# Kernel tuning notes

Measured on AMD Instinct MI355X. Metric: run time of the kernel, lower is better.

## Reference

```python
import jax, jax.numpy as jnp
import numpy as np

K = 32        # num_classes
NQ = 16384    # num query samples
C = 512       # feature_dim
H_REF = 512   # refinement_net hidden
H_CONF = 256  # confidence_net hidden
NUM_STEPS = 3


def setup_inputs() -> dict:
    key = jax.random.key(0)
    ks = jax.random.split(key, 8)
    s = 0.02
    return {
        "prototypes": jax.random.normal(ks[0], (K, C), jnp.float32),
        "query_features": jax.random.normal(ks[1], (NQ, C), jnp.float32),
        "query_distances": jax.random.uniform(ks[2], (NQ, K), jnp.float32) * 10.0,
        "W1": jax.random.normal(ks[3], (2 * C, H_REF), jnp.float32) * s,
        "b1": jnp.zeros((H_REF,), jnp.float32),
        "W2": jax.random.normal(ks[4], (H_REF, C), jnp.float32) * s,
        "b2": jnp.zeros((C,), jnp.float32),
        "Wc1": jax.random.normal(ks[5], (2 * C, H_CONF), jnp.float32) * s,
        "bc1": jnp.zeros((H_CONF,), jnp.float32),
        "Wc2": jax.random.normal(ks[6], (H_CONF, 1), jnp.float32) * s,
        "bc2": jnp.zeros((1,), jnp.float32),
    }


def reference(prototypes, query_features, query_distances,
              W1, b1, W2, b2, Wc1, bc1, Wc2, bc2):
    # ---- refinement loop (3 steps, sequential in refined prototypes) ----
    refined = prototypes
    for step in range(NUM_STEPS):
        # soft assignments over classes; temperature = step + 1
        soft = jax.nn.softmax(-query_distances / (step + 1.0), axis=-1)  # (NQ, K)
        wsum = jnp.maximum(soft.sum(axis=0), 1e-6)                       # (K,)  clamp(min=1e-6)
        wmean = (soft.T @ query_features) / wsum[:, None]                # (K, C)
        concat = jnp.concatenate([refined, wmean], axis=-1)              # (K, 2C)
        h = jax.nn.relu(concat @ W1 + b1)                                # dropout is identity in eval
        refinement = h @ W2 + b2                                         # (K, C)
        refined = refined + 0.1 * refinement

    # ---- confidence scores: MLP on [proto, query] pairs, mean over queries ----
    # Split first-layer weight into proto half and query half to avoid
    # materializing the (K, NQ, 2C) concat explicitly (same math).
    Wp, Wq = Wc1[:C], Wc1[C:]
    hp = prototypes @ Wp          # (K, H_CONF)
    hq = query_features @ Wq      # (NQ, H_CONF)
    hidden = jax.nn.relu(hp[:, None, :] + hq[None, :, :] + bc1)  # (K, NQ, H_CONF)
    conf = jax.nn.sigmoid(hidden @ Wc2 + bc2)                    # (K, NQ, 1)
    confidence_scores = conf.reshape(K, -1).mean(axis=1)         # (K,)

    return refined, confidence_scores
```

## Files before the change

kernel.cpp:

```cpp
#include <hip/hip_runtime.h>

#define KP 32
#define NQg 16384
#define CD 512
#define HC 256
#define NS 3

typedef __attribute__((ext_vector_type(8))) short short8;
typedef __attribute__((ext_vector_type(4))) short short4_t;
typedef __attribute__((ext_vector_type(8))) __bf16 bf16x8;
typedef __attribute__((ext_vector_type(4))) float floatx4;

union S8B8 { short8 s; bf16x8 b; };

__device__ __forceinline__ short f2bf(float f) {
    union { float f; unsigned u; } v; v.f = f;
    unsigned r = v.u + 0x7fffu + ((v.u >> 16) & 1u);
    return (short)(r >> 16);
}
__device__ __forceinline__ float bf2f(short s) {
    union { unsigned u; float f; } v; v.u = ((unsigned)(unsigned short)s) << 16;
    return v.f;
}
__device__ __forceinline__ float bflo(unsigned u) { return __uint_as_float(u << 16); }
__device__ __forceinline__ float bfhi(unsigned u) { return __uint_as_float(u & 0xffff0000u); }

__global__ __launch_bounds__(256) void k_A(const float* __restrict__ qd,
                                           const float* __restrict__ W1, const float* __restrict__ W2,
                                           const float* __restrict__ Wc1, const float* __restrict__ proto,
                                           const float* __restrict__ qf,
                                           short* __restrict__ softT,
                                           short* __restrict__ W1p, short* __restrict__ W2p,
                                           short* __restrict__ wqp, float* __restrict__ refined,
                                           short* __restrict__ qf2b, float* __restrict__ wmean,
                                           int* __restrict__ bar, float* __restrict__ dout) {
    int tid = threadIdx.x;
    int bid = blockIdx.x;
    if (bid < 64) {
        int q = bid * 256 + tid;
        float d[32];
        const float4* p = (const float4*)(qd + (size_t)q * 32);
#pragma unroll
        for (int j = 0; j < 8; j++) {
            float4 v = p[j];
            d[4 * j] = v.x; d[4 * j + 1] = v.y; d[4 * j + 2] = v.z; d[4 * j + 3] = v.w;
        }
#pragma unroll
        for (int s = 0; s < 3; s++) {
            float inv = -1.0f / (float)(s + 1);
            float e[32];
            float sum = 0.f;
#pragma unroll
            for (int k = 0; k < 32; k++) { e[k] = __expf(d[k] * inv); sum += e[k]; }
            float r = 1.0f / sum;
#pragma unroll
            for (int k = 0; k < 32; k++)
                softT[(size_t)(s * 32 + k) * NQg + q] = f2bf(e[k] * r);
        }
        return;
    }
    if (bid < 3712) {
        if (bid == 64) {
            if (tid < 32) dout[16384 + tid] = 0.f;
            else if (tid < 40) bar[tid - 32] = 0;
        }
        int idx = (bid - 64) * 256 + tid;
        if (idx < 524288) {
            int k = idx >> 9, n = idx & 511;
            W1p[((size_t)(k >> 3) * 512 + n) * 8 + (k & 7)] = f2bf(W1[idx]);
        } else if (idx < 786432) {
            int j = idx - 524288;
            int k = j >> 9, n = j & 511;
            W2p[((size_t)(k >> 3) * 512 + n) * 8 + (k & 7)] = f2bf(W2[j]);
        } else if (idx < 917504) {
            int j = idx - 786432;
            int k = j >> 8, n = j & 255;
            wqp[((size_t)(k >> 3) * 256 + n) * 8 + (k & 7)] = f2bf(Wc1[(size_t)(512 + k) * 256 + n]);
        } else {
            int j = idx - 917504;
            refined[j] = proto[j];
        }
        return;
    }
    if (bid < 3904) {
        int idx = (bid - 3712) * 256 + tid;
        wmean[idx] = 0.f;
        return;
    }
    {
#pragma unroll
        for (int it = 0; it < 4; it++) {
            int j = (bid - 3904) * 1024 + it * 256 + tid;
            float4 v = *(const float4*)&qf[(size_t)j * 4];
            short4_t o;
            o[0] = f2bf(v.x); o[1] = f2bf(v.y); o[2] = f2bf(v.z); o[3] = f2bf(v.w);
            *(short4_t*)&qf2b[(size_t)j * 4] = o;
        }
    }
}

__global__ __launch_bounds__(256) void k_B(const short* __restrict__ qf2b,
                                           const short* __restrict__ softT,
                                           const short* __restrict__ wqp,
                                           float* __restrict__ wmean,
                                           short* __restrict__ hq_g,
                                           float* __restrict__ wsuminv,
                                           const float* __restrict__ proto,
                                           const float* __restrict__ Wc1,
                                           const float* __restrict__ bc1,
                                           float* __restrict__ hpb) {
    __shared__ short B_lds[128 * 40];
    int tid = threadIdx.x;
    int lane = tid & 63, w = tid >> 6;
    int ml = lane & 15, q8 = lane >> 4;

    if (blockIdx.x < 256) {
        int kc = blockIdx.x >> 2, ns = blockIdx.x & 3;
        int c0 = ns * 128;
        int qbase0 = kc * 256;
        int c_l = 2 * lane;
        int q_l = 8 * w;

        floatx4 acc[6][2];
#pragma unroll
        for (int mt = 0; mt < 6; mt++)
#pragma unroll
            for (int nt = 0; nt < 2; nt++) acc[mt][nt] = (floatx4){0.f, 0.f, 0.f, 0.f};

        for (int step = 0; step < 8; step++) {
            int qb = qbase0 + step * 32;
            short8 sA, sB;
#pragma unroll
            for (int i = 0; i < 8; i++) {
                unsigned u = *(const unsigned*)&qf2b[(size_t)(qb + q_l + i) * 512 + c0 + c_l];
                sA[i] = (short)(u & 0xffffu);
                sB[i] = (short)(u >> 16);
            }
            __syncthreads();
            *(short8*)&B_lds[c_l * 40 + q_l] = sA;
            *(short8*)&B_lds[(c_l + 1) * 40 + q_l] = sB;
            S8B8 a[6];
#pragma unroll
            for (int mt = 0; mt < 6; mt++)
                a[mt].s = *(const short8*)&softT[(size_t)(mt * 16 + ml) * NQg + qb + q8 * 8];
            __syncthreads();
#pragma unroll
            for (int nt = 0; nt < 2; nt++) {
                S8B8 b; b.s = *(short8*)&B_lds[(w * 32 + nt * 16 + ml) * 40 + q8 * 8];
#pragma unroll
                for (int mt = 0; mt < 6; mt++)
                    acc[mt][nt] = __builtin_amdgcn_mfma_f32_16x16x32_bf16(a[mt].b, b.b, acc[mt][nt], 0, 0, 0);
            }
        }
#pragma unroll
        for (int mt = 0; mt < 6; mt++) {
#pragma unroll
            for (int nt = 0; nt < 2; nt++) {
                int c = c0 + w * 32 + nt * 16 + ml;
#pragma unroll
                for (int r = 0; r < 4; r++) {
                    int m = mt * 16 + q8 * 4 + r;
                    atomicAdd(&wmean[(size_t)m * 512 + c], acc[mt][nt][r]);
                }
            }
        }
    } else if (blockIdx.x < 512) {
        int m0 = (blockIdx.x - 256) * 64;
        int n0 = w * 64;
        floatx4 acc[4][4];
#pragma unroll
        for (int mt = 0; mt < 4; mt++)
#pragma unroll
            for (int nt = 0; nt < 4; nt++) acc[mt][nt] = (floatx4){0.f, 0.f, 0.f, 0.f};

#pragma unroll 4
        for (int kc = 0; kc < 512; kc += 32) {
            S8B8 a[4], b[4];
#pragma unroll
            for (int mt = 0; mt < 4; mt++)
                a[mt].s = *(const short8*)&qf2b[(size_t)(m0 + mt * 16 + ml) * 512 + kc + q8 * 8];
#pragma unroll
            for (int nt = 0; nt < 4; nt++)
                b[nt].s = *(const short8*)&wqp[((size_t)((kc >> 3) + q8) * 256 + n0 + nt * 16 + ml) * 8];
#pragma unroll
            for (int mt = 0; mt < 4; mt++)
#pragma unroll
                for (int nt = 0; nt < 4; nt++)
                    acc[mt][nt] = __builtin_amdgcn_mfma_f32_16x16x32_bf16(a[mt].b, b[nt].b, acc[mt][nt], 0, 0, 0);
        }
#pragma unroll
        for (int mt = 0; mt < 4; mt++)
#pragma unroll
            for (int nt = 0; nt < 4; nt++) {
                int col = n0 + nt * 16 + ml;
#pragma unroll
                for (int r = 0; r < 4; r++) {
                    int row = m0 + mt * 16 + q8 * 4 + r;
                    hq_g[(size_t)row * 256 + col] = f2bf(acc[mt][nt][r]);
                }
            }
    } else if (blockIdx.x < 608) {
        float* red = (float*)B_lds;
        int sk = blockIdx.x - 512;
        const short* row = softT + (size_t)sk * NQg;
        float s = 0.f;
#pragma unroll
        for (int j = 0; j < 8; j++) {
            short8 v = *(const short8*)&row[j * 2048 + tid * 8];
#pragma unroll
            for (int i = 0; i < 8; i++) s += bf2f(v[i]);
        }
        red[tid] = s;
        __syncthreads();
        for (int off = 128; off > 0; off >>= 1) {
            if (tid < off) red[tid] += red[tid + off];
            __syncthreads();
        }
        if (tid == 0) wsuminv[sk] = 1.0f / fmaxf(red[0], 1e-6f);
    } else {
        int r = blockIdx.x - 608;
        const float* pr = proto + r * 512;
        const float* wc = Wc1 + tid;
        float a0 = 0.f, a1 = 0.f, a2 = 0.f, a3 = 0.f;
#pragma unroll 4
        for (int i = 0; i < 512; i += 4) {
            float4 p4 = *(const float4*)&pr[i];
            float w0 = wc[(size_t)i * 256];
            float w1 = wc[(size_t)(i + 1) * 256];
            float w2 = wc[(size_t)(i + 2) * 256];
            float w3 = wc[(size_t)(i + 3) * 256];
            a0 += p4.x * w0;
            a1 += p4.y * w1;
            a2 += p4.z * w2;
            a3 += p4.w * w3;
        }
        hpb[r * 256 + tid] = bc1[tid] + ((a0 + a1) + (a2 + a3));
    }
}

__device__ __forceinline__ void gbar(int* bar, int phase, int nblk) {
    __syncthreads();
    if (threadIdx.x == 0) {
        __threadfence();
        __hip_atomic_fetch_add(&bar[phase], 1, __ATOMIC_ACQ_REL, __HIP_MEMORY_SCOPE_AGENT);
        while (__hip_atomic_load(&bar[phase], __ATOMIC_ACQUIRE, __HIP_MEMORY_SCOPE_AGENT) < nblk)
            __builtin_amdgcn_s_sleep(1);
    }
    __syncthreads();
}

__global__ __launch_bounds__(256) void k_D(const float* __restrict__ wmean,
                                           const float* __restrict__ wsuminv,
                                           const short* __restrict__ W1p,
                                           const float* __restrict__ b1,
                                           const short* __restrict__ W2p,
                                           const float* __restrict__ b2,
                                           float* __restrict__ refined,
                                           short* __restrict__ hb,
                                           int* __restrict__ bar,
                                           const short* __restrict__ hq_g,
                                           const float* __restrict__ hpb,
                                           const float* __restrict__ Wc2,
                                           const float* __restrict__ bc2p,
                                           float* __restrict__ dout) {
    __shared__ float smem[6688];
    int tid = threadIdx.x, lane = tid & 63, w = tid >> 6;
    int ml = lane & 15, q8 = lane >> 4;

    if (blockIdx.x < 16) {
        float (*red)[32][36] = (float(*)[32][36])smem;
        int nb = blockIdx.x;
        int phase = 0;
        for (int s = 0; s < 3; s++) {
            {
                const float* srcA = (w < 2) ? refined : (wmean + (size_t)s * 32 * 512 - 512);
                float iv0 = 1.f, iv1 = 1.f;
                if (w >= 2) {
                    iv0 = wsuminv[s * 32 + ml];
                    iv1 = wsuminv[s * 32 + 16 + ml];
                }
                int kw = w * 256;
                floatx4 acc[2][2];
#pragma unroll
                for (int mt = 0; mt < 2; mt++)
#pragma unroll
                    for (int nt = 0; nt < 2; nt++) acc[mt][nt] = (floatx4){0.f, 0.f, 0.f, 0.f};
                for (int st = 0; st < 8; st++) {
                    int k0 = kw + st * 32 + q8 * 8;
                    S8B8 a[2];
#pragma unroll
                    for (int mt = 0; mt < 2; mt++) {
                        float sc = mt ? iv1 : iv0;
                        const float* p = &srcA[(size_t)(mt * 16 + ml) * 512 + k0];
                        float4 f0 = *(const float4*)p;
                        float4 f1 = *(const float4*)(p + 4);
                        short8 t;
                        t[0] = f2bf(f0.x * sc); t[1] = f2bf(f0.y * sc);
                        t[2] = f2bf(f0.z * sc); t[3] = f2bf(f0.w * sc);
                        t[4] = f2bf(f1.x * sc); t[5] = f2bf(f1.y * sc);
                        t[6] = f2bf(f1.z * sc); t[7] = f2bf(f1.w * sc);
                        a[mt].s = t;
                    }
#pragma unroll
                    for (int nt = 0; nt < 2; nt++) {
                        int n = nb * 32 + nt * 16 + ml;
                        S8B8 b; b.s = *(const short8*)&W1p[((size_t)(k0 >> 3) * 512 + n) * 8];
#pragma unroll
                        for (int mt = 0; mt < 2; mt++)
                            acc[mt][nt] = __builtin_amdgcn_mfma_f32_16x16x32_bf16(a[mt].b, b.b, acc[mt][nt], 0, 0, 0);
                    }
                }
                __syncthreads();
#pragma unroll
                for (int mt = 0; mt < 2; mt++)
#pragma unroll
                    for (int nt = 0; nt < 2; nt++)
#pragma unroll
                        for (int r = 0; r < 4; r++)
                            red[w][mt * 16 + q8 * 4 + r][nt * 16 + ml] = acc[mt][nt][r];
                __syncthreads();
                int m = tid >> 3, n0 = (tid & 7) * 4;
                short4_t o;
#pragma unroll
                for (int i = 0; i < 4; i++) {
                    float v = b1[nb * 32 + n0 + i];
#pragma unroll
                    for (int w4 = 0; w4 < 4; w4++) v += red[w4][m][n0 + i];
                    o[i] = f2bf(fmaxf(v, 0.f));
                }
                *(short4_t*)&hb[(size_t)m * 512 + nb * 32 + n0] = o;
            }
            gbar(bar, phase++, 16);
            {
                int kw = w * 128;
                floatx4 acc[2][2];
#pragma unroll
                for (int mt = 0; mt < 2; mt++)
#pragma unroll
                    for (int nt = 0; nt < 2; nt++) acc[mt][nt] = (floatx4){0.f, 0.f, 0.f, 0.f};
                for (int st = 0; st < 4; st++) {
                    int k0 = kw + st * 32 + q8 * 8;
                    S8B8 a[2];
#pragma unroll
                    for (int mt = 0; mt < 2; mt++)
                        a[mt].s = *(const short8*)&hb[(size_t)(mt * 16 + ml) * 512 + k0];
#pragma unroll
                    for (int nt = 0; nt < 2; nt++) {
                        int n = nb * 32 + nt * 16 + ml;
                        S8B8 b; b.s = *(const short8*)&W2p[((size_t)(k0 >> 3) * 512 + n) * 8];
#pragma unroll
                        for (int mt = 0; mt < 2; mt++)
                            acc[mt][nt] = __builtin_amdgcn_mfma_f32_16x16x32_bf16(a[mt].b, b.b, acc[mt][nt], 0, 0, 0);
                    }
                }
                __syncthreads();
#pragma unroll
                for (int mt = 0; mt < 2; mt++)
#pragma unroll
                    for (int nt = 0; nt < 2; nt++)
#pragma unroll
                        for (int r = 0; r < 4; r++)
                            red[w][mt * 16 + q8 * 4 + r][nt * 16 + ml] = acc[mt][nt][r];
                __syncthreads();
                int m = tid >> 3, n0 = (tid & 7) * 4;
#pragma unroll
                for (int i = 0; i < 4; i++) {
                    int c = nb * 32 + n0 + i;
                    float v = b2[c];
#pragma unroll
                    for (int w4 = 0; w4 < 4; w4++) v += red[w4][m][n0 + i];
                    float val = refined[(size_t)m * 512 + c] + 0.1f * v;
                    refined[(size_t)m * 512 + c] = val;
                    if (s == 2) dout[(size_t)m * 512 + c] = val;
                }
            }
            if (s < 2) gbar(bar, phase++, 16);
        }
    } else {
        short* hq_lds = (short*)smem;
        short* hp_s   = (short*)smem + 4480;
        float* wc2s   = smem + 6400;
        float* confl  = smem + 6656;
        int q0 = (blockIdx.x - 16) * 16;

        wc2s[tid] = Wc2[tid];
        if (tid < 32) confl[tid] = 0.f;
#pragma unroll
        for (int i = 0; i < 8; i++) {
            int idx = i * 256 + tid;
            int r = idx >> 6, c = (idx & 63) * 4;
            float4 v = *(const float4*)&hpb[r * 256 + c];
            short4_t o;
            o[0] = f2bf(v.x); o[1] = f2bf(v.y); o[2] = f2bf(v.z); o[3] = f2bf(v.w);
            *(short4_t*)&hp_s[r * 260 + c] = o;
        }
        {
            const short* hqs = hq_g + (size_t)q0 * 256;
            int r = tid >> 4, c = (tid & 15) * 16;
            *(short8*)&hq_lds[r * 280 + c] = *(const short8*)&hqs[r * 256 + c];
            *(short8*)&hq_lds[r * 280 + c + 8] = *(const short8*)&hqs[r * 256 + c + 8];
        }
        __syncthreads();

        int q = tid & 15, kg = tid >> 4;
        int k0 = kg, k1 = kg + 16;
        float s0 = 0.f, s1 = 0.f;
        for (int h = 0; h < 256; h += 4) {
            uint2 hv = *(uint2*)&hq_lds[q * 280 + h];
            float f0 = bflo(hv.x), f1 = bfhi(hv.x), f2 = bflo(hv.y), f3 = bfhi(hv.y);
            uint2 u0 = *(uint2*)&hp_s[k0 * 260 + h];
            uint2 u1 = *(uint2*)&hp_s[k1 * 260 + h];
            float4 wv = *(float4*)&wc2s[h];
            s0 += fmaxf(bflo(u0.x) + f0, 0.f) * wv.x;
            s0 += fmaxf(bfhi(u0.x) + f1, 0.f) * wv.y;
            s0 += fmaxf(bflo(u0.y) + f2, 0.f) * wv.z;
            s0 += fmaxf(bfhi(u0.y) + f3, 0.f) * wv.w;
            s1 += fmaxf(bflo(u1.x) + f0, 0.f) * wv.x;
            s1 += fmaxf(bfhi(u1.x) + f1, 0.f) * wv.y;
            s1 += fmaxf(bflo(u1.y) + f2, 0.f) * wv.z;
            s1 += fmaxf(bfhi(u1.y) + f3, 0.f) * wv.w;
        }
        float bc2 = bc2p[0];
        float v0 = 1.f / (1.f + __expf(-(s0 + bc2)));
        float v1 = 1.f / (1.f + __expf(-(s1 + bc2)));
        atomicAdd(&confl[k0], v0);
        atomicAdd(&confl[k1], v1);
        __syncthreads();
        if (tid < 32) atomicAdd(&dout[16384 + tid], confl[tid] * (1.0f / 16384.0f));
    }
}

extern "C" void kernel_launch(void* const* d_in, const int* in_sizes, int n_in,
                              void* d_out, int out_size, void* d_ws, size_t ws_size,
                              hipStream_t stream) {
    const float* proto = (const float*)d_in[0];
    const float* qf    = (const float*)d_in[1];
    const float* qd    = (const float*)d_in[2];
    const float* W1    = (const float*)d_in[3];
    const float* b1    = (const float*)d_in[4];
    const float* W2    = (const float*)d_in[5];
    const float* b2    = (const float*)d_in[6];
    const float* Wc1   = (const float*)d_in[7];
    const float* bc1   = (const float*)d_in[8];
    const float* Wc2   = (const float*)d_in[9];
    const float* bc2   = (const float*)d_in[10];
    float* out = (float*)d_out;

    float* ws = (float*)d_ws;
    short* softT   = (short*)ws;
    short* qf2b    = (short*)(ws + 786432);
    float* wmean   = ws + 4980736;
    float* refined = ws + 5029888;
    short* hb      = (short*)(ws + 5046272);
    short* W1p     = (short*)(ws + 5054464);
    short* W2p     = (short*)(ws + 5316608);
    short* wqp     = (short*)(ws + 5447680);
    float* hpb     = ws + 5513216;
    int*   bar     = (int*)(ws + 5521408);
    float* wsuminv = ws + 5521416;
    short* hq      = (short*)(ws + 5521536);

    k_A<<<5952, 256, 0, stream>>>(qd, W1, W2, Wc1, proto, qf, softT, W1p, W2p, wqp,
                                  refined, qf2b, wmean, bar, out);
    k_B<<<640, 256, 0, stream>>>(qf2b, softT, wqp, wmean, hq, wsuminv, proto, Wc1, bc1, hpb);
    k_D<<<1040, 256, 0, stream>>>(wmean, wsuminv, W1p, b1, W2p, b2, refined, hb, bar,
                                  hq, hpb, Wc2, bc2, out);
}
```

Measured before the change: 172.8 us.

## Restructure refinement MLP split, move hp to k_A, smaller hq tiles

The hp prototype projection moves from k_B into k_A. The hq GEMM tiles shrink from 64 to 32 rows, giving more blocks. In the refinement blocks of k_D, each wave now computes a full-K 16x16 output tile instead of a K-split that needed an LDS reduction. This relies on pre-converted bf16 copies of wmean (scaled by wsuminv, with an extra grid barrier) and of the refined prototypes. The aim is to remove the LDS reduction, the syncthreads and the per-step fp32-to-bf16 conversions from the sequential critical path, in exchange for longer per-wave K loops and an extra barrier.

```diff
diff --git a/kernel.cpp b/kernel.cpp
--- a/kernel.cpp
+++ b/kernel.cpp
@@ -28,11 +28,13 @@
 __global__ __launch_bounds__(256) void k_A(const float* __restrict__ qd,
                                            const float* __restrict__ W1, const float* __restrict__ W2,
                                            const float* __restrict__ Wc1, const float* __restrict__ proto,
-                                           const float* __restrict__ qf,
+                                           const float* __restrict__ qf, const float* __restrict__ bc1,
                                            short* __restrict__ softT,
                                            short* __restrict__ W1p, short* __restrict__ W2p,
                                            short* __restrict__ wqp, float* __restrict__ refined,
+                                           short* __restrict__ refined_b,
                                            short* __restrict__ qf2b, float* __restrict__ wmean,
+                                           float* __restrict__ hpb,
                                            int* __restrict__ bar, float* __restrict__ dout) {
     int tid = threadIdx.x;
     int bid = blockIdx.x;
@@ -78,7 +80,9 @@
             wqp[((size_t)(k >> 3) * 256 + n) * 8 + (k & 7)] = f2bf(Wc1[(size_t)(512 + k) * 256 + n]);
         } else {
             int j = idx - 917504;
-            refined[j] = proto[j];
+            float v = proto[j];
+            refined[j] = v;
+            refined_b[j] = f2bf(v);
         }
         return;
     }
@@ -87,7 +91,7 @@
         wmean[idx] = 0.f;
         return;
     }
-    {
+    if (bid < 5952) {
 #pragma unroll
         for (int it = 0; it < 4; it++) {
             int j = (bid - 3904) * 1024 + it * 256 + tid;
@@ -96,129 +100,10 @@
             o[0] = f2bf(v.x); o[1] = f2bf(v.y); o[2] = f2bf(v.z); o[3] = f2bf(v.w);
             *(short4_t*)&qf2b[(size_t)j * 4] = o;
         }
-    }
-}
-
-__global__ __launch_bounds__(256) void k_B(const short* __restrict__ qf2b,
-                                           const short* __restrict__ softT,
-                                           const short* __restrict__ wqp,
-                                           float* __restrict__ wmean,
-                                           short* __restrict__ hq_g,
-                                           float* __restrict__ wsuminv,
-                                           const float* __restrict__ proto,
-                                           const float* __restrict__ Wc1,
-                                           const float* __restrict__ bc1,
-                                           float* __restrict__ hpb) {
-    __shared__ short B_lds[128 * 40];
-    int tid = threadIdx.x;
-    int lane = tid & 63, w = tid >> 6;
-    int ml = lane & 15, q8 = lane >> 4;
-
-    if (blockIdx.x < 256) {
-        int kc = blockIdx.x >> 2, ns = blockIdx.x & 3;
-        int c0 = ns * 128;
-        int qbase0 = kc * 256;
-        int c_l = 2 * lane;
-        int q_l = 8 * w;
-
-        floatx4 acc[6][2];
-#pragma unroll
-        for (int mt = 0; mt < 6; mt++)
-#pragma unroll
-            for (int nt = 0; nt < 2; nt++) acc[mt][nt] = (floatx4){0.f, 0.f, 0.f, 0.f};
-
-        for (int step = 0; step < 8; step++) {
-            int qb = qbase0 + step * 32;
-            short8 sA, sB;
-#pragma unroll
-            for (int i = 0; i < 8; i++) {
-                unsigned u = *(const unsigned*)&qf2b[(size_t)(qb + q_l + i) * 512 + c0 + c_l];
-                sA[i] = (short)(u & 0xffffu);
-                sB[i] = (short)(u >> 16);
-            }
-            __syncthreads();
-            *(short8*)&B_lds[c_l * 40 + q_l] = sA;
-            *(short8*)&B_lds[(c_l + 1) * 40 + q_l] = sB;
-            S8B8 a[6];
-#pragma unroll
-            for (int mt = 0; mt < 6; mt++)
-                a[mt].s = *(const short8*)&softT[(size_t)(mt * 16 + ml) * NQg + qb + q8 * 8];
-            __syncthreads();
-#pragma unroll
-            for (int nt = 0; nt < 2; nt++) {
-                S8B8 b; b.s = *(short8*)&B_lds[(w * 32 + nt * 16 + ml) * 40 + q8 * 8];
-#pragma unroll
-                for (int mt = 0; mt < 6; mt++)
-                    acc[mt][nt] = __builtin_amdgcn_mfma_f32_16x16x32_bf16(a[mt].b, b.b, acc[mt][nt], 0, 0, 0);
-            }
-        }
-#pragma unroll
-        for (int mt = 0; mt < 6; mt++) {
-#pragma unroll
-            for (int nt = 0; nt < 2; nt++) {
-                int c = c0 + w * 32 + nt * 16 + ml;
-#pragma unroll
-                for (int r = 0; r < 4; r++) {
-                    int m = mt * 16 + q8 * 4 + r;
-                    atomicAdd(&wmean[(size_t)m * 512 + c], acc[mt][nt][r]);
-                }
-            }
-        }
-    } else if (blockIdx.x < 512) {
-        int m0 = (blockIdx.x - 256) * 64;
-        int n0 = w * 64;
-        floatx4 acc[4][4];
-#pragma unroll
-        for (int mt = 0; mt < 4; mt++)
-#pragma unroll
-            for (int nt = 0; nt < 4; nt++) acc[mt][nt] = (floatx4){0.f, 0.f, 0.f, 0.f};
-
-#pragma unroll 4
-        for (int kc = 0; kc < 512; kc += 32) {
-            S8B8 a[4], b[4];
-#pragma unroll
-            for (int mt = 0; mt < 4; mt++)
-                a[mt].s = *(const short8*)&qf2b[(size_t)(m0 + mt * 16 + ml) * 512 + kc + q8 * 8];
-#pragma unroll
-            for (int nt = 0; nt < 4; nt++)
-                b[nt].s = *(const short8*)&wqp[((size_t)((kc >> 3) + q8) * 256 + n0 + nt * 16 + ml) * 8];
-#pragma unroll
-            for (int mt = 0; mt < 4; mt++)
-#pragma unroll
-                for (int nt = 0; nt < 4; nt++)
-                    acc[mt][nt] = __builtin_amdgcn_mfma_f32_16x16x32_bf16(a[mt].b, b[nt].b, acc[mt][nt], 0, 0, 0);
-        }
-#pragma unroll
-        for (int mt = 0; mt < 4; mt++)
-#pragma unroll
-            for (int nt = 0; nt < 4; nt++) {
-                int col = n0 + nt * 16 + ml;
-#pragma unroll
-                for (int r = 0; r < 4; r++) {
-                    int row = m0 + mt * 16 + q8 * 4 + r;
-                    hq_g[(size_t)row * 256 + col] = f2bf(acc[mt][nt][r]);
-                }
-            }
-    } else if (blockIdx.x < 608) {
-        float* red = (float*)B_lds;
-        int sk = blockIdx.x - 512;
-        const short* row = softT + (size_t)sk * NQg;
-        float s = 0.f;
-#pragma unroll
-        for (int j = 0; j < 8; j++) {
-            short8 v = *(const short8*)&row[j * 2048 + tid * 8];
-#pragma unroll
-            for (int i = 0; i < 8; i++) s += bf2f(v[i]);
-        }
-        red[tid] = s;
-        __syncthreads();
-        for (int off = 128; off > 0; off >>= 1) {
-            if (tid < off) red[tid] += red[tid + off];
-            __syncthreads();
-        }
-        if (tid == 0) wsuminv[sk] = 1.0f / fmaxf(red[0], 1e-6f);
-    } else {
-        int r = blockIdx.x - 608;
+        return;
+    }
+    {
+        int r = bid - 5952;
         const float* pr = proto + r * 512;
         const float* wc = Wc1 + tid;
         float a0 = 0.f, a1 = 0.f, a2 = 0.f, a3 = 0.f;
@@ -238,6 +123,123 @@
     }
 }
 
+__global__ __launch_bounds__(256) void k_B(const short* __restrict__ qf2b,
+                                           const short* __restrict__ softT,
+                                           const short* __restrict__ wqp,
+                                           float* __restrict__ wmean,
+                                           short* __restrict__ hq_g,
+                                           float* __restrict__ wsuminv) {
+    __shared__ short B_lds[128 * 40];
+    int tid = threadIdx.x;
+    int lane = tid & 63, w = tid >> 6;
+    int ml = lane & 15, q8 = lane >> 4;
+
+    if (blockIdx.x < 256) {
+        int kc = blockIdx.x >> 2, ns = blockIdx.x & 3;
+        int c0 = ns * 128;
+        int qbase0 = kc * 256;
+        int c_l = 2 * lane;
+        int q_l = 8 * w;
+
+        floatx4 acc[6][2];
+#pragma unroll
+        for (int mt = 0; mt < 6; mt++)
+#pragma unroll
+            for (int nt = 0; nt < 2; nt++) acc[mt][nt] = (floatx4){0.f, 0.f, 0.f, 0.f};
+
+        for (int step = 0; step < 8; step++) {
+            int qb = qbase0 + step * 32;
+            short8 sA, sB;
+#pragma unroll
+            for (int i = 0; i < 8; i++) {
+                unsigned u = *(const unsigned*)&qf2b[(size_t)(qb + q_l + i) * 512 + c0 + c_l];
+                sA[i] = (short)(u & 0xffffu);
+                sB[i] = (short)(u >> 16);
+            }
+            __syncthreads();
+            *(short8*)&B_lds[c_l * 40 + q_l] = sA;
+            *(short8*)&B_lds[(c_l + 1) * 40 + q_l] = sB;
+            S8B8 a[6];
+#pragma unroll
+            for (int mt = 0; mt < 6; mt++)
+                a[mt].s = *(const short8*)&softT[(size_t)(mt * 16 + ml) * NQg + qb + q8 * 8];
+            __syncthreads();
+#pragma unroll
+            for (int nt = 0; nt < 2; nt++) {
+                S8B8 b; b.s = *(short8*)&B_lds[(w * 32 + nt * 16 + ml) * 40 + q8 * 8];
+#pragma unroll
+                for (int mt = 0; mt < 6; mt++)
+                    acc[mt][nt] = __builtin_amdgcn_mfma_f32_16x16x32_bf16(a[mt].b, b.b, acc[mt][nt], 0, 0, 0);
+            }
+        }
+#pragma unroll
+        for (int mt = 0; mt < 6; mt++) {
+#pragma unroll
+            for (int nt = 0; nt < 2; nt++) {
+                int c = c0 + w * 32 + nt * 16 + ml;
+#pragma unroll
+                for (int r = 0; r < 4; r++) {
+                    int m = mt * 16 + q8 * 4 + r;
+                    atomicAdd(&wmean[(size_t)m * 512 + c], acc[mt][nt][r]);
+                }
+            }
+        }
+    } else if (blockIdx.x < 768) {
+        int m0 = (blockIdx.x - 256) * 32;
+        int n0 = w * 64;
+        floatx4 acc[2][4];
+#pragma unroll
+        for (int mt = 0; mt < 2; mt++)
+#pragma unroll
+            for (int nt = 0; nt < 4; nt++) acc[mt][nt] = (floatx4){0.f, 0.f, 0.f, 0.f};
+
+#pragma unroll 4
+        for (int kc = 0; kc < 512; kc += 32) {
+            S8B8 a[2], b[4];
+#pragma unroll
+            for (int mt = 0; mt < 2; mt++)
+                a[mt].s = *(const short8*)&qf2b[(size_t)(m0 + mt * 16 + ml) * 512 + kc + q8 * 8];
+#pragma unroll
+            for (int nt = 0; nt < 4; nt++)
+                b[nt].s = *(const short8*)&wqp[((size_t)((kc >> 3) + q8) * 256 + n0 + nt * 16 + ml) * 8];
+#pragma unroll
+            for (int mt = 0; mt < 2; mt++)
+#pragma unroll
+                for (int nt = 0; nt < 4; nt++)
+                    acc[mt][nt] = __builtin_amdgcn_mfma_f32_16x16x32_bf16(a[mt].b, b[nt].b, acc[mt][nt], 0, 0, 0);
+        }
+#pragma unroll
+        for (int mt = 0; mt < 2; mt++)
+#pragma unroll
+            for (int nt = 0; nt < 4; nt++) {
+                int col = n0 + nt * 16 + ml;
+#pragma unroll
+                for (int r = 0; r < 4; r++) {
+                    int row = m0 + mt * 16 + q8 * 4 + r;
+                    hq_g[(size_t)row * 256 + col] = f2bf(acc[mt][nt][r]);
+                }
+            }
+    } else {
+        float* red = (float*)B_lds;
+        int sk = blockIdx.x - 768;
+        const short* row = softT + (size_t)sk * NQg;
+        float s = 0.f;
+#pragma unroll
+        for (int j = 0; j < 8; j++) {
+            short8 v = *(const short8*)&row[j * 2048 + tid * 8];
+#pragma unroll
+            for (int i = 0; i < 8; i++) s += bf2f(v[i]);
+        }
+        red[tid] = s;
+        __syncthreads();
+        for (int off = 128; off > 0; off >>= 1) {
+            if (tid < off) red[tid] += red[tid + off];
+            __syncthreads();
+        }
+        if (tid == 0) wsuminv[sk] = 1.0f / fmaxf(red[0], 1e-6f);
+    }
+}
+
 __device__ __forceinline__ void gbar(int* bar, int phase, int nblk) {
     __syncthreads();
     if (threadIdx.x == 0) {
@@ -262,116 +264,71 @@
                                            const float* __restrict__ hpb,
                                            const float* __restrict__ Wc2,
                                            const float* __restrict__ bc2p,
-                                           float* __restrict__ dout) {
+                                           float* __restrict__ dout,
+                                           short* __restrict__ wmean_b,
+                                           short* __restrict__ refined_b) {
     __shared__ float smem[6688];
     int tid = threadIdx.x, lane = tid & 63, w = tid >> 6;
     int ml = lane & 15, q8 = lane >> 4;
 
     if (blockIdx.x < 16) {
-        float (*red)[32][36] = (float(*)[32][36])smem;
         int nb = blockIdx.x;
+        int nh = w & 1, mh = w >> 1;
+        int n = nb * 32 + nh * 16 + ml;
         int phase = 0;
+
+#pragma unroll
+        for (int i = 0; i < 12; i++) {
+            int idx = i * 4096 + nb * 256 + tid;
+            int row = idx >> 9;
+            wmean_b[idx] = f2bf(wmean[idx] * wsuminv[row]);
+        }
+        gbar(bar, phase++, 16);
+
         for (int s = 0; s < 3; s++) {
             {
-                const float* srcA = (w < 2) ? refined : (wmean + (size_t)s * 32 * 512 - 512);
-                float iv0 = 1.f, iv1 = 1.f;
-                if (w >= 2) {
-                    iv0 = wsuminv[s * 32 + ml];
-                    iv1 = wsuminv[s * 32 + 16 + ml];
-                }
-                int kw = w * 256;
-                floatx4 acc[2][2];
-#pragma unroll
-                for (int mt = 0; mt < 2; mt++)
-#pragma unroll
-                    for (int nt = 0; nt < 2; nt++) acc[mt][nt] = (floatx4){0.f, 0.f, 0.f, 0.f};
-                for (int st = 0; st < 8; st++) {
-                    int k0 = kw + st * 32 + q8 * 8;
-                    S8B8 a[2];
-#pragma unroll
-                    for (int mt = 0; mt < 2; mt++) {
-                        float sc = mt ? iv1 : iv0;
-                        const float* p = &srcA[(size_t)(mt * 16 + ml) * 512 + k0];
-                        float4 f0 = *(const float4*)p;
-                        float4 f1 = *(const float4*)(p + 4);
-                        short8 t;
-                        t[0] = f2bf(f0.x * sc); t[1] = f2bf(f0.y * sc);
-                        t[2] = f2bf(f0.z * sc); t[3] = f2bf(f0.w * sc);
-                        t[4] = f2bf(f1.x * sc); t[5] = f2bf(f1.y * sc);
-                        t[6] = f2bf(f1.z * sc); t[7] = f2bf(f1.w * sc);
-                        a[mt].s = t;
-                    }
-#pragma unroll
-                    for (int nt = 0; nt < 2; nt++) {
-                        int n = nb * 32 + nt * 16 + ml;
-                        S8B8 b; b.s = *(const short8*)&W1p[((size_t)(k0 >> 3) * 512 + n) * 8];
-#pragma unroll
-                        for (int mt = 0; mt < 2; mt++)
-                            acc[mt][nt] = __builtin_amdgcn_mfma_f32_16x16x32_bf16(a[mt].b, b.b, acc[mt][nt], 0, 0, 0);
-                    }
-                }
-                __syncthreads();
-#pragma unroll
-                for (int mt = 0; mt < 2; mt++)
-#pragma unroll
-                    for (int nt = 0; nt < 2; nt++)
-#pragma unroll
-                        for (int r = 0; r < 4; r++)
-                            red[w][mt * 16 + q8 * 4 + r][nt * 16 + ml] = acc[mt][nt][r];
-                __syncthreads();
-                int m = tid >> 3, n0 = (tid & 7) * 4;
-                short4_t o;
-#pragma unroll
-                for (int i = 0; i < 4; i++) {
-                    float v = b1[nb * 32 + n0 + i];
-#pragma unroll
-                    for (int w4 = 0; w4 < 4; w4++) v += red[w4][m][n0 + i];
-                    o[i] = f2bf(fmaxf(v, 0.f));
-                }
-                *(short4_t*)&hb[(size_t)m * 512 + nb * 32 + n0] = o;
+                const short* rfb = refined_b + (size_t)(mh * 16 + ml) * 512;
+                const short* wmb = wmean_b + (size_t)(s * 32 + mh * 16 + ml) * 512;
+                floatx4 acc = (floatx4){0.f, 0.f, 0.f, 0.f};
+#pragma unroll
+                for (int st = 0; st < 16; st++) {
+                    int k0 = st * 32 + q8 * 8;
+                    S8B8 a; a.s = *(const short8*)&rfb[k0];
+                    S8B8 b; b.s = *(const short8*)&W1p[((size_t)(k0 >> 3) * 512 + n) * 8];
+                    acc = __builtin_amdgcn_mfma_f32_16x16x32_bf16(a.b, b.b, acc, 0, 0, 0);
+                }
+#pragma unroll
+                for (int st = 16; st < 32; st++) {
+                    int k0 = st * 32 + q8 * 8;
+                    S8B8 a; a.s = *(const short8*)&wmb[k0 - 512];
+                    S8B8 b; b.s = *(const short8*)&W1p[((size_t)(k0 >> 3) * 512 + n) * 8];
+                    acc = __builtin_amdgcn_mfma_f32_16x16x32_bf16(a.b, b.b, acc, 0, 0, 0);
+                }
+                float bias = b1[n];
+#pragma unroll
+                for (int r = 0; r < 4; r++) {
+                    int row = mh * 16 + q8 * 4 + r;
+                    hb[(size_t)row * 512 + n] = f2bf(fmaxf(acc[r] + bias, 0.f));
+                }
             }
             gbar(bar, phase++, 16);
             {
-                int kw = w * 128;
-                floatx4 acc[2][2];
-#pragma unroll
-                for (int mt = 0; mt < 2; mt++)
-#pragma unroll
-                    for (int nt = 0; nt < 2; nt++) acc[mt][nt] = (floatx4){0.f, 0.f, 0.f, 0.f};
-                for (int st = 0; st < 4; st++) {
-                    int k0 = kw + st * 32 + q8 * 8;
-                    S8B8 a[2];
-#pragma unroll
-                    for (int mt = 0; mt < 2; mt++)
-                        a[mt].s = *(const short8*)&hb[(size_t)(mt * 16 + ml) * 512 + k0];
-#pragma unroll
-                    for (int nt = 0; nt < 2; nt++) {
-                        int n = nb * 32 + nt * 16 + ml;
-                        S8B8 b; b.s = *(const short8*)&W2p[((size_t)(k0 >> 3) * 512 + n) * 8];
-#pragma unroll
-                        for (int mt = 0; mt < 2; mt++)
-                            acc[mt][nt] = __builtin_amdgcn_mfma_f32_16x16x32_bf16(a[mt].b, b.b, acc[mt][nt], 0, 0, 0);
-                    }
-                }
-                __syncthreads();
-#pragma unroll
-                for (int mt = 0; mt < 2; mt++)
-#pragma unroll
-                    for (int nt = 0; nt < 2; nt++)
-#pragma unroll
-                        for (int r = 0; r < 4; r++)
-                            red[w][mt * 16 + q8 * 4 + r][nt * 16 + ml] = acc[mt][nt][r];
-                __syncthreads();
-                int m = tid >> 3, n0 = (tid & 7) * 4;
-#pragma unroll
-                for (int i = 0; i < 4; i++) {
-                    int c = nb * 32 + n0 + i;
-                    float v = b2[c];
-#pragma unroll
-                    for (int w4 = 0; w4 < 4; w4++) v += red[w4][m][n0 + i];
-                    float val = refined[(size_t)m * 512 + c] + 0.1f * v;
-                    refined[(size_t)m * 512 + c] = val;
-                    if (s == 2) dout[(size_t)m * 512 + c] = val;
+                floatx4 acc = (floatx4){0.f, 0.f, 0.f, 0.f};
+#pragma unroll
+                for (int st = 0; st < 16; st++) {
+                    int k0 = st * 32 + q8 * 8;
+                    S8B8 a; a.s = *(const short8*)&hb[(size_t)(mh * 16 + ml) * 512 + k0];
+                    S8B8 b; b.s = *(const short8*)&W2p[((size_t)(k0 >> 3) * 512 + n) * 8];
+                    acc = __builtin_amdgcn_mfma_f32_16x16x32_bf16(a.b, b.b, acc, 0, 0, 0);
+                }
+                float b2v = b2[n];
+#pragma unroll
+                for (int r = 0; r < 4; r++) {
+                    int row = mh * 16 + q8 * 4 + r;
+                    float val = refined[(size_t)row * 512 + n] + 0.1f * (acc[r] + b2v);
+                    refined[(size_t)row * 512 + n] = val;
+                    refined_b[(size_t)row * 512 + n] = f2bf(val);
+                    if (s == 2) dout[(size_t)row * 512 + n] = val;
                 }
             }
             if (s < 2) gbar(bar, phase++, 16);
@@ -459,10 +416,12 @@
     int*   bar     = (int*)(ws + 5521408);
     float* wsuminv = ws + 5521416;
     short* hq      = (short*)(ws + 5521536);
-
-    k_A<<<5952, 256, 0, stream>>>(qd, W1, W2, Wc1, proto, qf, softT, W1p, W2p, wqp,
-                                  refined, qf2b, wmean, bar, out);
-    k_B<<<640, 256, 0, stream>>>(qf2b, softT, wqp, wmean, hq, wsuminv, proto, Wc1, bc1, hpb);
+    short* refined_b = (short*)(ws + 7618688);
+    short* wmean_b   = (short*)(ws + 7626880);
+
+    k_A<<<5984, 256, 0, stream>>>(qd, W1, W2, Wc1, proto, qf, bc1, softT, W1p, W2p, wqp,
+                                  refined, refined_b, qf2b, wmean, hpb, bar, out);
+    k_B<<<864, 256, 0, stream>>>(qf2b, softT, wqp, wmean, hq, wsuminv);
     k_D<<<1040, 256, 0, stream>>>(wmean, wsuminv, W1p, b1, W2p, b2, refined, hb, bar,
-                                  hq, hpb, Wc2, bc2, out);
-}
+                                  hq, hpb, Wc2, bc2, out, wmean_b, refined_b);
+}
```

Result: slower. 194.1 us (+12.3%).

## Fuse softmax and bf16 conversion into consumers, drop global softT and qf2b

Applied to the files above, without the earlier changes.

The softmax over distances is now computed per block directly into LDS inside the wmean GEMM kernel, so the global softT buffer and its separate column-sum pass go away. Column sums are accumulated with atomics into wsum. The query-feature bf16 copy is removed: the wmean GEMM and the confidence kernel read fp32 query features and convert them on the fly. The hq projection is computed inside the confidence blocks instead of in a separate stage. The intent is to cut global memory round trips and kernel work, at the cost of recomputing the softmax in 4 blocks per query chunk and redoing the conversion in each consumer.

```diff
diff --git a/kernel.cpp b/kernel.cpp
--- a/kernel.cpp
+++ b/kernel.cpp
@@ -1,10 +1,4 @@
 #include <hip/hip_runtime.h>
-
-#define KP 32
-#define NQg 16384
-#define CD 512
-#define HC 256
-#define NS 3
 
 typedef __attribute__((ext_vector_type(8))) short short8;
 typedef __attribute__((ext_vector_type(4))) short short4_t;
@@ -25,200 +19,17 @@
 __device__ __forceinline__ float bflo(unsigned u) { return __uint_as_float(u << 16); }
 __device__ __forceinline__ float bfhi(unsigned u) { return __uint_as_float(u & 0xffff0000u); }
 
-__global__ __launch_bounds__(256) void k_A(const float* __restrict__ qd,
-                                           const float* __restrict__ W1, const float* __restrict__ W2,
+__global__ __launch_bounds__(256) void k_A(const float* __restrict__ W1, const float* __restrict__ W2,
                                            const float* __restrict__ Wc1, const float* __restrict__ proto,
-                                           const float* __restrict__ qf,
-                                           short* __restrict__ softT,
+                                           const float* __restrict__ bc1,
                                            short* __restrict__ W1p, short* __restrict__ W2p,
                                            short* __restrict__ wqp, float* __restrict__ refined,
-                                           short* __restrict__ qf2b, float* __restrict__ wmean,
-                                           int* __restrict__ bar, float* __restrict__ dout) {
-    int tid = threadIdx.x;
-    int bid = blockIdx.x;
-    if (bid < 64) {
-        int q = bid * 256 + tid;
-        float d[32];
-        const float4* p = (const float4*)(qd + (size_t)q * 32);
-#pragma unroll
-        for (int j = 0; j < 8; j++) {
-            float4 v = p[j];
-            d[4 * j] = v.x; d[4 * j + 1] = v.y; d[4 * j + 2] = v.z; d[4 * j + 3] = v.w;
-        }
-#pragma unroll
-        for (int s = 0; s < 3; s++) {
-            float inv = -1.0f / (float)(s + 1);
-            float e[32];
-            float sum = 0.f;
-#pragma unroll
-            for (int k = 0; k < 32; k++) { e[k] = __expf(d[k] * inv); sum += e[k]; }
-            float r = 1.0f / sum;
-#pragma unroll
-            for (int k = 0; k < 32; k++)
-                softT[(size_t)(s * 32 + k) * NQg + q] = f2bf(e[k] * r);
-        }
-        return;
-    }
-    if (bid < 3712) {
-        if (bid == 64) {
-            if (tid < 32) dout[16384 + tid] = 0.f;
-            else if (tid < 40) bar[tid - 32] = 0;
-        }
-        int idx = (bid - 64) * 256 + tid;
-        if (idx < 524288) {
-            int k = idx >> 9, n = idx & 511;
-            W1p[((size_t)(k >> 3) * 512 + n) * 8 + (k & 7)] = f2bf(W1[idx]);
-        } else if (idx < 786432) {
-            int j = idx - 524288;
-            int k = j >> 9, n = j & 511;
-            W2p[((size_t)(k >> 3) * 512 + n) * 8 + (k & 7)] = f2bf(W2[j]);
-        } else if (idx < 917504) {
-            int j = idx - 786432;
-            int k = j >> 8, n = j & 255;
-            wqp[((size_t)(k >> 3) * 256 + n) * 8 + (k & 7)] = f2bf(Wc1[(size_t)(512 + k) * 256 + n]);
-        } else {
-            int j = idx - 917504;
-            refined[j] = proto[j];
-        }
-        return;
-    }
-    if (bid < 3904) {
-        int idx = (bid - 3712) * 256 + tid;
-        wmean[idx] = 0.f;
-        return;
-    }
-    {
-#pragma unroll
-        for (int it = 0; it < 4; it++) {
-            int j = (bid - 3904) * 1024 + it * 256 + tid;
-            float4 v = *(const float4*)&qf[(size_t)j * 4];
-            short4_t o;
-            o[0] = f2bf(v.x); o[1] = f2bf(v.y); o[2] = f2bf(v.z); o[3] = f2bf(v.w);
-            *(short4_t*)&qf2b[(size_t)j * 4] = o;
-        }
-    }
-}
-
-__global__ __launch_bounds__(256) void k_B(const short* __restrict__ qf2b,
-                                           const short* __restrict__ softT,
-                                           const short* __restrict__ wqp,
-                                           float* __restrict__ wmean,
-                                           short* __restrict__ hq_g,
-                                           float* __restrict__ wsuminv,
-                                           const float* __restrict__ proto,
-                                           const float* __restrict__ Wc1,
-                                           const float* __restrict__ bc1,
-                                           float* __restrict__ hpb) {
-    __shared__ short B_lds[128 * 40];
-    int tid = threadIdx.x;
-    int lane = tid & 63, w = tid >> 6;
-    int ml = lane & 15, q8 = lane >> 4;
-
-    if (blockIdx.x < 256) {
-        int kc = blockIdx.x >> 2, ns = blockIdx.x & 3;
-        int c0 = ns * 128;
-        int qbase0 = kc * 256;
-        int c_l = 2 * lane;
-        int q_l = 8 * w;
-
-        floatx4 acc[6][2];
-#pragma unroll
-        for (int mt = 0; mt < 6; mt++)
-#pragma unroll
-            for (int nt = 0; nt < 2; nt++) acc[mt][nt] = (floatx4){0.f, 0.f, 0.f, 0.f};
-
-        for (int step = 0; step < 8; step++) {
-            int qb = qbase0 + step * 32;
-            short8 sA, sB;
-#pragma unroll
-            for (int i = 0; i < 8; i++) {
-                unsigned u = *(const unsigned*)&qf2b[(size_t)(qb + q_l + i) * 512 + c0 + c_l];
-                sA[i] = (short)(u & 0xffffu);
-                sB[i] = (short)(u >> 16);
-            }
-            __syncthreads();
-            *(short8*)&B_lds[c_l * 40 + q_l] = sA;
-            *(short8*)&B_lds[(c_l + 1) * 40 + q_l] = sB;
-            S8B8 a[6];
-#pragma unroll
-            for (int mt = 0; mt < 6; mt++)
-                a[mt].s = *(const short8*)&softT[(size_t)(mt * 16 + ml) * NQg + qb + q8 * 8];
-            __syncthreads();
-#pragma unroll
-            for (int nt = 0; nt < 2; nt++) {
-                S8B8 b; b.s = *(short8*)&B_lds[(w * 32 + nt * 16 + ml) * 40 + q8 * 8];
-#pragma unroll
-                for (int mt = 0; mt < 6; mt++)
-                    acc[mt][nt] = __builtin_amdgcn_mfma_f32_16x16x32_bf16(a[mt].b, b.b, acc[mt][nt], 0, 0, 0);
-            }
-        }
-#pragma unroll
-        for (int mt = 0; mt < 6; mt++) {
-#pragma unroll
-            for (int nt = 0; nt < 2; nt++) {
-                int c = c0 + w * 32 + nt * 16 + ml;
-#pragma unroll
-                for (int r = 0; r < 4; r++) {
-                    int m = mt * 16 + q8 * 4 + r;
-                    atomicAdd(&wmean[(size_t)m * 512 + c], acc[mt][nt][r]);
-                }
-            }
-        }
-    } else if (blockIdx.x < 512) {
-        int m0 = (blockIdx.x - 256) * 64;
-        int n0 = w * 64;
-        floatx4 acc[4][4];
-#pragma unroll
-        for (int mt = 0; mt < 4; mt++)
-#pragma unroll
-            for (int nt = 0; nt < 4; nt++) acc[mt][nt] = (floatx4){0.f, 0.f, 0.f, 0.f};
-
-#pragma unroll 4
-        for (int kc = 0; kc < 512; kc += 32) {
-            S8B8 a[4], b[4];
-#pragma unroll
-            for (int mt = 0; mt < 4; mt++)
-                a[mt].s = *(const short8*)&qf2b[(size_t)(m0 + mt * 16 + ml) * 512 + kc + q8 * 8];
-#pragma unroll
-            for (int nt = 0; nt < 4; nt++)
-                b[nt].s = *(const short8*)&wqp[((size_t)((kc >> 3) + q8) * 256 + n0 + nt * 16 + ml) * 8];
-#pragma unroll
-            for (int mt = 0; mt < 4; mt++)
-#pragma unroll
-                for (int nt = 0; nt < 4; nt++)
-                    acc[mt][nt] = __builtin_amdgcn_mfma_f32_16x16x32_bf16(a[mt].b, b[nt].b, acc[mt][nt], 0, 0, 0);
-        }
-#pragma unroll
-        for (int mt = 0; mt < 4; mt++)
-#pragma unroll
-            for (int nt = 0; nt < 4; nt++) {
-                int col = n0 + nt * 16 + ml;
-#pragma unroll
-                for (int r = 0; r < 4; r++) {
-                    int row = m0 + mt * 16 + q8 * 4 + r;
-                    hq_g[(size_t)row * 256 + col] = f2bf(acc[mt][nt][r]);
-                }
-            }
-    } else if (blockIdx.x < 608) {
-        float* red = (float*)B_lds;
-        int sk = blockIdx.x - 512;
-        const short* row = softT + (size_t)sk * NQg;
-        float s = 0.f;
-#pragma unroll
-        for (int j = 0; j < 8; j++) {
-            short8 v = *(const short8*)&row[j * 2048 + tid * 8];
-#pragma unroll
-            for (int i = 0; i < 8; i++) s += bf2f(v[i]);
-        }
-        red[tid] = s;
-        __syncthreads();
-        for (int off = 128; off > 0; off >>= 1) {
-            if (tid < off) red[tid] += red[tid + off];
-            __syncthreads();
-        }
-        if (tid == 0) wsuminv[sk] = 1.0f / fmaxf(red[0], 1e-6f);
-    } else {
-        int r = blockIdx.x - 608;
+                                           float* __restrict__ wmean, float* __restrict__ hpb,
+                                           int* __restrict__ bar, float* __restrict__ wsum,
+                                           float* __restrict__ dout) {
+    int tid = threadIdx.x, bid = blockIdx.x;
+    if (bid < 32) {
+        int r = bid;
         const float* pr = proto + r * 512;
         const float* wc = Wc1 + tid;
         float a0 = 0.f, a1 = 0.f, a2 = 0.f, a3 = 0.f;
@@ -235,6 +46,139 @@
             a3 += p4.w * w3;
         }
         hpb[r * 256 + tid] = bc1[tid] + ((a0 + a1) + (a2 + a3));
+        return;
+    }
+    if (bid < 480) {
+        int idx = (bid - 32) * 256 + tid;
+        if (idx < 65536) {
+            int kg = idx >> 9, n = idx & 511;
+            short8 o;
+#pragma unroll
+            for (int j = 0; j < 8; j++) o[j] = f2bf(W1[(size_t)(kg * 8 + j) * 512 + n]);
+            *(short8*)&W1p[((size_t)kg * 512 + n) * 8] = o;
+        } else if (idx < 98304) {
+            int j2 = idx - 65536;
+            int kg = j2 >> 9, n = j2 & 511;
+            short8 o;
+#pragma unroll
+            for (int j = 0; j < 8; j++) o[j] = f2bf(W2[(size_t)(kg * 8 + j) * 512 + n]);
+            *(short8*)&W2p[((size_t)kg * 512 + n) * 8] = o;
+        } else {
+            int j3 = idx - 98304;
+            int kg = j3 >> 8, n = j3 & 255;
+            short8 o;
+#pragma unroll
+            for (int j = 0; j < 8; j++) o[j] = f2bf(Wc1[(size_t)(512 + kg * 8 + j) * 256 + n]);
+            *(short8*)&wqp[((size_t)kg * 256 + n) * 8] = o;
+        }
+        return;
+    }
+    if (bid < 544) {
+        int idx = (bid - 480) * 256 + tid;
+        refined[idx] = proto[idx];
+        return;
+    }
+    if (bid < 736) {
+        int idx = (bid - 544) * 256 + tid;
+        wmean[idx] = 0.f;
+        return;
+    }
+    {
+        if (tid < 96) wsum[tid] = 0.f;
+        else if (tid < 104) bar[tid - 96] = 0;
+        else if (tid >= 128 && tid < 160) dout[16384 + tid - 128] = 0.f;
+    }
+}
+
+__global__ __launch_bounds__(256) void k_B(const float* __restrict__ qd, const float* __restrict__ qf,
+                                           float* __restrict__ wmean, float* __restrict__ wsum) {
+    __shared__ short soft_lds[96 * 264];
+    __shared__ short B_lds[128 * 40];
+    int tid = threadIdx.x;
+    int kc = blockIdx.x >> 2, ns = blockIdx.x & 3;
+    int qb0 = kc * 256, c0 = ns * 128;
+
+    {
+        float d[32];
+        const float4* p = (const float4*)(qd + (size_t)(qb0 + tid) * 32);
+#pragma unroll
+        for (int j = 0; j < 8; j++) {
+            float4 v = p[j];
+            d[4 * j] = v.x; d[4 * j + 1] = v.y; d[4 * j + 2] = v.z; d[4 * j + 3] = v.w;
+        }
+#pragma unroll
+        for (int s = 0; s < 3; s++) {
+            float inv = -1.0f / (float)(s + 1);
+            float e[32];
+            float sum = 0.f;
+#pragma unroll
+            for (int k = 0; k < 32; k++) { e[k] = __expf(d[k] * inv); sum += e[k]; }
+            float r = 1.0f / sum;
+#pragma unroll
+            for (int k = 0; k < 32; k++)
+                soft_lds[(s * 32 + k) * 264 + tid] = f2bf(e[k] * r);
+        }
+    }
+    __syncthreads();
+
+    if (ns == 0 && tid < 96) {
+        const short* row = &soft_lds[tid * 264];
+        float ssum = 0.f;
+#pragma unroll 4
+        for (int j = 0; j < 32; j++) {
+            short8 v = *(const short8*)&row[j * 8];
+#pragma unroll
+            for (int i = 0; i < 8; i++) ssum += bf2f(v[i]);
+        }
+        atomicAdd(&wsum[tid], ssum);
+    }
+
+    int lane = tid & 63, w = tid >> 6;
+    int ml = lane & 15, q8 = lane >> 4;
+    int c_l = 2 * lane, q_l = 8 * w;
+
+    floatx4 acc[6][2];
+#pragma unroll
+    for (int mt = 0; mt < 6; mt++)
+#pragma unroll
+        for (int nt = 0; nt < 2; nt++) acc[mt][nt] = (floatx4){0.f, 0.f, 0.f, 0.f};
+
+    for (int step = 0; step < 8; step++) {
+        int qb = step * 32;
+        short8 sA, sB;
+#pragma unroll
+        for (int i = 0; i < 8; i++) {
+            float2 u = *(const float2*)&qf[(size_t)(qb0 + qb + q_l + i) * 512 + c0 + c_l];
+            sA[i] = f2bf(u.x);
+            sB[i] = f2bf(u.y);
+        }
+        __syncthreads();
+        *(short8*)&B_lds[c_l * 40 + q_l] = sA;
+        *(short8*)&B_lds[(c_l + 1) * 40 + q_l] = sB;
+        S8B8 a[6];
+#pragma unroll
+        for (int mt = 0; mt < 6; mt++)
+            a[mt].s = *(const short8*)&soft_lds[(mt * 16 + ml) * 264 + qb + q8 * 8];
+        __syncthreads();
+#pragma unroll
+        for (int nt = 0; nt < 2; nt++) {
+            S8B8 b; b.s = *(short8*)&B_lds[(w * 32 + nt * 16 + ml) * 40 + q8 * 8];
+#pragma unroll
+            for (int mt = 0; mt < 6; mt++)
+                acc[mt][nt] = __builtin_amdgcn_mfma_f32_16x16x32_bf16(a[mt].b, b.b, acc[mt][nt], 0, 0, 0);
+        }
+    }
+#pragma unroll
+    for (int mt = 0; mt < 6; mt++) {
+#pragma unroll
+        for (int nt = 0; nt < 2; nt++) {
+            int c = c0 + w * 32 + nt * 16 + ml;
+#pragma unroll
+            for (int r = 0; r < 4; r++) {
+                int m = mt * 16 + q8 * 4 + r;
+                atomicAdd(&wmean[(size_t)m * 512 + c], acc[mt][nt][r]);
+            }
+        }
     }
 }
 
@@ -250,7 +194,7 @@
 }
 
 __global__ __launch_bounds__(256) void k_D(const float* __restrict__ wmean,
-                                           const float* __restrict__ wsuminv,
+                                           const float* __restrict__ wsum,
                                            const short* __restrict__ W1p,
                                            const float* __restrict__ b1,
                                            const short* __restrict__ W2p,
@@ -258,7 +202,8 @@
                                            float* __restrict__ refined,
                                            short* __restrict__ hb,
                                            int* __restrict__ bar,
-                                           const short* __restrict__ hq_g,
+                                           const float* __restrict__ qf,
+                                           const short* __restrict__ wqp,
                                            const float* __restrict__ hpb,
                                            const float* __restrict__ Wc2,
                                            const float* __restrict__ bc2p,
@@ -276,8 +221,8 @@
                 const float* srcA = (w < 2) ? refined : (wmean + (size_t)s * 32 * 512 - 512);
                 float iv0 = 1.f, iv1 = 1.f;
                 if (w >= 2) {
-                    iv0 = wsuminv[s * 32 + ml];
-                    iv1 = wsuminv[s * 32 + 16 + ml];
+                    iv0 = 1.f / fmaxf(wsum[s * 32 + ml], 1e-6f);
+                    iv1 = 1.f / fmaxf(wsum[s * 32 + 16 + ml], 1e-6f);
                 }
                 int kw = w * 256;
                 floatx4 acc[2][2];
@@ -395,10 +340,30 @@
             *(short4_t*)&hp_s[r * 260 + c] = o;
         }
         {
-            const short* hqs = hq_g + (size_t)q0 * 256;
-            int r = tid >> 4, c = (tid & 15) * 16;
-            *(short8*)&hq_lds[r * 280 + c] = *(const short8*)&hqs[r * 256 + c];
-            *(short8*)&hq_lds[r * 280 + c + 8] = *(const short8*)&hqs[r * 256 + c + 8];
+            floatx4 acc[4];
+#pragma unroll
+            for (int nt = 0; nt < 4; nt++) acc[nt] = (floatx4){0.f, 0.f, 0.f, 0.f};
+            const float* qfa = qf + (size_t)(q0 + ml) * 512 + q8 * 8;
+#pragma unroll 4
+            for (int kc = 0; kc < 512; kc += 32) {
+                float4 fa = *(const float4*)&qfa[kc];
+                float4 fb = *(const float4*)&qfa[kc + 4];
+                short8 t;
+                t[0] = f2bf(fa.x); t[1] = f2bf(fa.y); t[2] = f2bf(fa.z); t[3] = f2bf(fa.w);
+                t[4] = f2bf(fb.x); t[5] = f2bf(fb.y); t[6] = f2bf(fb.z); t[7] = f2bf(fb.w);
+                S8B8 a; a.s = t;
+#pragma unroll
+                for (int nt = 0; nt < 4; nt++) {
+                    int col = w * 64 + nt * 16 + ml;
+                    S8B8 b; b.s = *(const short8*)&wqp[((size_t)((kc >> 3) + q8) * 256 + col) * 8];
+                    acc[nt] = __builtin_amdgcn_mfma_f32_16x16x32_bf16(a.b, b.b, acc[nt], 0, 0, 0);
+                }
+            }
+#pragma unroll
+            for (int nt = 0; nt < 4; nt++)
+#pragma unroll
+                for (int r = 0; r < 4; r++)
+                    hq_lds[(q8 * 4 + r) * 280 + w * 64 + nt * 16 + ml] = f2bf(acc[nt][r]);
         }
         __syncthreads();
 
@@ -447,22 +412,19 @@
     float* out = (float*)d_out;
 
     float* ws = (float*)d_ws;
-    short* softT   = (short*)ws;
-    short* qf2b    = (short*)(ws + 786432);
-    float* wmean   = ws + 4980736;
-    float* refined = ws + 5029888;
-    short* hb      = (short*)(ws + 5046272);
-    short* W1p     = (short*)(ws + 5054464);
-    short* W2p     = (short*)(ws + 5316608);
-    short* wqp     = (short*)(ws + 5447680);
-    float* hpb     = ws + 5513216;
-    int*   bar     = (int*)(ws + 5521408);
-    float* wsuminv = ws + 5521416;
-    short* hq      = (short*)(ws + 5521536);
-
-    k_A<<<5952, 256, 0, stream>>>(qd, W1, W2, Wc1, proto, qf, softT, W1p, W2p, wqp,
-                                  refined, qf2b, wmean, bar, out);
-    k_B<<<640, 256, 0, stream>>>(qf2b, softT, wqp, wmean, hq, wsuminv, proto, Wc1, bc1, hpb);
-    k_D<<<1040, 256, 0, stream>>>(wmean, wsuminv, W1p, b1, W2p, b2, refined, hb, bar,
-                                  hq, hpb, Wc2, bc2, out);
-}
+    float* wmean   = ws;
+    float* refined = ws + 49152;
+    short* hb      = (short*)(ws + 65536);
+    short* W1p     = (short*)(ws + 73728);
+    short* W2p     = (short*)(ws + 335872);
+    short* wqp     = (short*)(ws + 466944);
+    float* hpb     = ws + 532480;
+    int*   bar     = (int*)(ws + 540672);
+    float* wsum    = ws + 540680;
+
+    k_A<<<737, 256, 0, stream>>>(W1, W2, Wc1, proto, bc1, W1p, W2p, wqp,
+                                 refined, wmean, hpb, bar, wsum, out);
+    k_B<<<256, 256, 0, stream>>>(qd, qf, wmean, wsum);
+    k_D<<<1040, 256, 0, stream>>>(wmean, wsum, W1p, b1, W2p, b2, refined, hb, bar,
+                                  qf, wqp, hpb, Wc2, bc2, out);
+}
```

Measured after the change: 180.3 us. 4.3% more time.
